# Kernel optimization log

Hardware: AMD Instinct MI355X
Metric: run time of the kernel (lower is better)

The kernel has to match this reference:

```python
import jax, jax.numpy as jnp
import numpy as np

V, E, S, TT, H, C, B = 50000, 300, 128, 12, 512, 3, 128


def setup_inputs() -> dict:
    key = jax.random.key(0)
    ks = jax.random.split(key, 12)
    sc = lambda n: 1.0 / np.sqrt(n)
    return {
        "target_ids": jax.random.randint(ks[0], (B, TT), 0, V),
        "target_len": jax.random.randint(ks[1], (B,), 1, TT + 1, dtype=jnp.int32),
        "left_ids": jax.random.randint(ks[2], (B, S), 0, V),
        "left_len": jax.random.randint(ks[3], (B,), 1, S + 1, dtype=jnp.int32),
        "right_ids": jax.random.randint(ks[4], (B, S), 0, V),
        "right_len": jax.random.randint(ks[5], (B,), 1, S + 1, dtype=jnp.int32),
        "embeddings": jax.random.normal(ks[6], (V, E), jnp.float32) * 0.1,
        "W_left": jax.random.normal(ks[7], (2 * E + H, 4 * H), jnp.float32) * sc(2 * E + H),
        "b_left": jnp.zeros((4 * H,), jnp.float32),
        "W_right": jax.random.normal(ks[8], (2 * E + H, 4 * H), jnp.float32) * sc(2 * E + H),
        "b_right": jnp.zeros((4 * H,), jnp.float32),
        "W_dense": jax.random.normal(ks[9], (2 * H, C), jnp.float32) * sc(2 * H),
        "b_dense": jnp.zeros((C,), jnp.float32),
    }


def _lstm_last_state(x, lens, W, b):
    # x: [B,S,D] inputs, lens: [B]; TF BasicLSTMCell gate order (i, j, f, o), forget_bias=1.0.
    # dynamic_rnn(sequence_length=lens): state frozen once t >= len.
    b_, s_, _ = x.shape
    xs = jnp.swapaxes(x, 0, 1)  # [S,B,D]
    step_mask = jnp.arange(s_)[:, None] < lens[None, :]  # [S,B]
    h0 = jnp.zeros((b_, H), x.dtype)
    c0 = jnp.zeros((b_, H), x.dtype)

    def step(carry, inp):
        h, c = carry
        x_t, m_t = inp
        z = jnp.concatenate([x_t, h], axis=-1) @ W + b  # [B,4H]
        i, j, f, o = jnp.split(z, 4, axis=-1)
        c_new = jax.nn.sigmoid(f + 1.0) * c + jax.nn.sigmoid(i) * jnp.tanh(j)
        h_new = jax.nn.sigmoid(o) * jnp.tanh(c_new)
        m = m_t[:, None]
        return (jnp.where(m, h_new, h), jnp.where(m, c_new, c)), None

    (h, _c), _ = jax.lax.scan(step, (h0, c0), (xs, step_mask))
    return h


def reference(target_ids, target_len, left_ids, left_len, right_ids, right_len,
              embeddings, W_left, b_left, W_right, b_right, W_dense, b_dense):
    # mean target embedding over valid target tokens (variable_len_batch_mean)
    tgt = embeddings[target_ids]  # [B,TT,E]
    tmask = (jnp.arange(TT)[None, :] < target_len[:, None]).astype(tgt.dtype)
    mean_t = jnp.sum(tgt * tmask[:, :, None], axis=1) / target_len[:, None].astype(tgt.dtype)  # [B,E]

    def ctx_inputs(ids):
        e = embeddings[ids]  # [B,S,E]
        # stack([emb, mean_t], axis=2) then reshape -> per-timestep concat [emb_t, mean_t]
        return jnp.concatenate([e, jnp.broadcast_to(mean_t[:, None, :], e.shape)], axis=-1)  # [B,S,2E]

    h_l = _lstm_last_state(ctx_inputs(left_ids), left_len, W_left, b_left)
    h_r = _lstm_last_state(ctx_inputs(right_ids), right_len, W_right, b_right)
    logits = jnp.concatenate([h_l, h_r], axis=-1) @ W_dense + b_dense  # [B,C]
    return logits
```

## Files before the change

kernel.cpp:

```cpp
#include <hip/hip_runtime.h>

#define NB 128
#define NS 128
#define NT 12
#define NE 300
#define NH 512
#define NCOL 2048
#define WGSC __HIP_MEMORY_SCOPE_WORKGROUP

typedef _Float16 h8v __attribute__((ext_vector_type(8)));
typedef __attribute__((ext_vector_type(4))) float f4v;
typedef __attribute__((ext_vector_type(4))) int   i4v;

__device__ __forceinline__ unsigned short f2h(float f) {
  union { _Float16 h; unsigned short u; } c; c.h = (_Float16)f; return c.u;
}
__device__ __forceinline__ float sigm(float x) { return 1.f / (1.f + __expf(-x)); }
__device__ __forceinline__ float tanh_(float x) { const float e = __expf(2.f * x); return 1.f - 2.f / (e + 1.f); }

__device__ __forceinline__ unsigned packh(float a, float b, int tag) {
  unsigned lo = f2h(a), hi = f2h(b);
  lo = (lo & ~1u) | (unsigned)(tag & 1);
  hi = (hi & ~1u) | (unsigned)((tag >> 1) & 1);
  return lo | (hi << 16);
}

__device__ __forceinline__ void st32f_uc(float* p, float v) {
  asm volatile("global_store_dword %0, %1, off sc1" :: "v"(p), "v"(v) : "memory");
}
__device__ __forceinline__ void st32i_uc(int* p, int v) {
  asm volatile("global_store_dword %0, %1, off sc1" :: "v"(p), "v"(v) : "memory");
}
__device__ __forceinline__ void st32u_uc(unsigned* p, unsigned v) {
  asm volatile("global_store_dword %0, %1, off sc1" :: "v"(p), "v"(v) : "memory");
}
__device__ __forceinline__ int ldflag(const int* p) {
  int v;
  asm volatile("global_load_dword %0, %1, off sc1\n\ts_waitcnt vmcnt(0)" : "=v"(v) : "v"(p) : "memory");
  return v;
}
__device__ __forceinline__ void ld64_uc(const char* a, i4v* r) {
  asm volatile(
    "global_load_dwordx4 %0, %4, off sc1\n\t"
    "global_load_dwordx4 %1, %4, off offset:16 sc1\n\t"
    "global_load_dwordx4 %2, %4, off offset:32 sc1\n\t"
    "global_load_dwordx4 %3, %4, off offset:48 sc1\n\t"
    "s_waitcnt vmcnt(0)"
    : "=&v"(r[0]), "=&v"(r[1]), "=&v"(r[2]), "=&v"(r[3])
    : "v"(a) : "memory");
}

struct Params {
  const int *tids, *tlen, *lids, *llen, *rids, *rlen;
  const float *emb, *Wl, *bl, *Wr, *br, *Wd, *bd;
  float* out;
  unsigned short* hbuf;
  float* hfin;
  int* bar;
};

__device__ __forceinline__ void lspin(int* c, int tgt) {
  while (__hip_atomic_load(c, __ATOMIC_RELAXED, WGSC) < tgt) {}
  __builtin_amdgcn_fence(__ATOMIC_ACQUIRE, "workgroup");
}
__device__ __forceinline__ void lspin_s(int* c, int tgt) {
  while (__hip_atomic_load(c, __ATOMIC_RELAXED, WGSC) < tgt)
    __builtin_amdgcn_s_sleep(1);
  __builtin_amdgcn_fence(__ATOMIC_ACQUIRE, "workgroup");
}
__device__ __forceinline__ void larrive(int* c) {
  __hip_atomic_fetch_add(c, 1, __ATOMIC_ACQ_REL, WGSC);
}

#define OFF_HS   0
#define OFF_XS   16384
#define OFF_ZX   26624
#define OFF_ZS   51200
#define OFF_WTH  51200
#define OFF_WTX  34816
#define LDS_SZ   59392

__global__ __launch_bounds__(512, 1) void lstm_all(Params p) {
  __shared__ __align__(16) char lds[LDS_SZ];
  __shared__ int lenL[16];
  __shared__ float redL[8][4];
  __shared__ int cnt[8];

  const int tid = threadIdx.x;
  const int wid = blockIdx.x;
  if (tid < 8) cnt[tid] = 0;

  const int g = wid & 15, ht = wid >> 4;
  const int side = g & 1, bt = g >> 1;
  const int b0 = bt * 16, d0c = ht * 32;
  const int* lenp = side ? p.rlen : p.llen;
  const int* gids = side ? p.rids : p.lids;
  const float* W = side ? p.Wr : p.Wl;
  const float* bias = side ? p.br : p.bl;
  int* fl = p.bar + g * 1024;

  const bool isH = tid < 256;
  const int wv = tid >> 6;
  const int ln = tid & 63;
  const int lwv = isH ? wv : (wv - 4);
  const int kgrp = ln >> 4;
  const int stid = tid & 255;

  float* meanTT = (float*)lds;
  float* zS = (float*)(lds + OFF_ZS);

  {
    const int r = tid >> 5, l32 = tid & 31;
    const int b = b0 + r;
    const int Lt = p.tlen[b];
    const float inv = 1.f / (float)Lt;
    int toks[NT];
    #pragma unroll
    for (int t = 0; t < NT; ++t) toks[t] = p.tids[b * NT + t];
    for (int k = l32; k < NE; k += 32) {
      float s = 0.f;
      #pragma unroll
      for (int t = 0; t < NT; ++t)
        if (t < Lt) s += p.emb[(size_t)toks[t] * NE + k];
      meanTT[k * 16 + r] = s * inv;
    }
    if (tid < 16) lenL[tid] = lenp[b0 + tid];
  }
  __syncthreads();

  if (isH) {
    const int row_c = stid >> 4;
    const int m = stid & 15;

    float zb1[4], zb2[4];
    {
      #pragma unroll
      for (int gq = 0; gq < 4; ++gq) {
        const float* wp = W + (size_t)NE * NCOL + gq * NH + d0c;
        float a1 = bias[gq * NH + d0c + 2 * m];
        float a2 = bias[gq * NH + d0c + 2 * m + 1];
        for (int k = 0; k < NE; ++k) {
          const float mv = meanTT[k * 16 + row_c];
          a1 += mv * wp[(size_t)k * NCOL + 2 * m];
          a2 += mv * wp[(size_t)k * NCOL + 2 * m + 1];
        }
        zb1[gq] = a1; zb2[gq] = a2;
      }
    }
    if (ln == 0) larrive(&cnt[6]);

    int he = 0;
    auto hpbar = [&]() {
      ++he;
      if (ln == 0) larrive(&cnt[7]);
      while (__hip_atomic_load(&cnt[7], __ATOMIC_RELAXED, WGSC) < 4 * he) {}
      __builtin_amdgcn_fence(__ATOMIC_ACQUIRE, "workgroup");
    };
    h8v hfr0[16], hfr1[16];
    {
      unsigned short* wT = (unsigned short*)(lds + OFF_WTH);
      const int r3 = stid >> 3;
      const int part = stid & 7;
      const int gate_p = part >> 1, half_p = part & 1;
      for (int i = 0; i < 16; ++i) {
        const int k = 600 + i * 32 + r3;
        const float* wr = W + (size_t)k * NCOL + gate_p * NH + d0c + half_p * 16;
        const f4v a0 = *(const f4v*)wr;
        const f4v a1 = *(const f4v*)(wr + 4);
        const f4v a2 = *(const f4v*)(wr + 8);
        const f4v a3 = *(const f4v*)(wr + 12);
        #pragma unroll
        for (int j = 0; j < 4; ++j) {
          wT[(part * 16 + j) * 32 + r3]      = f2h(a0[j]);
          wT[(part * 16 + 4 + j) * 32 + r3]  = f2h(a1[j]);
          wT[(part * 16 + 8 + j) * 32 + r3]  = f2h(a2[j]);
          wT[(part * 16 + 12 + j) * 32 + r3] = f2h(a3[j]);
        }
        hpbar();
        const int c0 = lwv * 32 + (ln & 15);
        hfr0[i] = *(const h8v*)((char*)wT + c0 * 64 + kgrp * 16);
        hfr1[i] = *(const h8v*)((char*)wT + (c0 + 16) * 64 + kgrp * 16);
        hpbar();
      }
    }

    float cR1 = 0.f, cR2 = 0.f, hR1 = 0.f, hR2 = 0.f;
    const int a_r = ln & 15;
    const int srow = stid >> 4;
    const int schk = stid & 15;
    for (int t = 0; t < NS; ++t) {
      lspin(&cnt[2], 4 * (t + 1));
      const float* zx = (const float*)(lds + OFF_ZX + (t % 3) * 8192);
      f4v acc0, acc1;
      #pragma unroll
      for (int rg = 0; rg < 4; ++rg) {
        const int rr = kgrp * 4 + rg;
        acc0[rg] = zx[rr * 128 + lwv * 32 + (ln & 15)];
        acc1[rg] = zx[rr * 128 + lwv * 32 + 16 + (ln & 15)];
      }
      if (ln == 0) larrive(&cnt[3]);

      if (t) {
        const char* src = (const char*)(p.hbuf
            + (size_t)(((t & 1) * 2 + side) * NB + b0 + srow) * NH + schk * 32);
        const unsigned exp32 = ((unsigned)(t & 1)) | (((unsigned)((t >> 1) & 1)) << 16);
        i4v v[4];
        for (;;) {
          ld64_uc(src, v);
          unsigned bad = 0;
          #pragma unroll
          for (int q = 0; q < 4; ++q)
            #pragma unroll
            for (int j = 0; j < 4; ++j)
              bad |= (((unsigned)v[q][j]) ^ exp32) & 0x00010001u;
          if (!bad) break;
        }
        #pragma unroll
        for (int q = 0; q < 4; ++q) {
          const int c16 = schk * 4 + q;
          *(i4v*)(lds + OFF_HS + srow * 1024 + ((c16 * 16) ^ ((srow & 7) << 4))) = v[q];
        }
        if (ln == 0) larrive(&cnt[0]);
        while (__hip_atomic_load(&cnt[0], __ATOMIC_RELAXED, WGSC) < 4 * t) {}
        __builtin_amdgcn_fence(__ATOMIC_ACQUIRE, "workgroup");
        #pragma unroll
        for (int kt = 0; kt < 16; ++kt) {
          h8v a = *(const h8v*)(lds + OFF_HS + a_r * 1024
                                + (((kt * 4 + kgrp) * 16) ^ ((a_r & 7) << 4)));
          acc0 = __builtin_amdgcn_mfma_f32_16x16x32_f16(a, hfr0[kt], acc0, 0, 0, 0);
          acc1 = __builtin_amdgcn_mfma_f32_16x16x32_f16(a, hfr1[kt], acc1, 0, 0, 0);
        }
      }

      #pragma unroll
      for (int rg = 0; rg < 4; ++rg) {
        const int rr = kgrp * 4 + rg;
        zS[rr * 128 + lwv * 32 + (ln & 15)]      = acc0[rg];
        zS[rr * 128 + lwv * 32 + 16 + (ln & 15)] = acc1[rg];
      }
      if (ln == 0) larrive(&cnt[4]);
      while (__hip_atomic_load(&cnt[4], __ATOMIC_RELAXED, WGSC) < 4 * (t + 1)) {}
      __builtin_amdgcn_fence(__ATOMIC_ACQUIRE, "workgroup");

      {
        const float* zr = zS + row_c * 128;
        float zi = zr[0 * 32 + 2 * m] + zb1[0], zj = zr[1 * 32 + 2 * m] + zb1[1];
        float zf = zr[2 * 32 + 2 * m] + zb1[2], zo = zr[3 * 32 + 2 * m] + zb1[3];
        float ig = sigm(zi), jg = tanh_(zj), fg = sigm(zf + 1.f), og = sigm(zo);
        float cn = fg * cR1 + ig * jg;
        float hn = og * tanh_(cn);
        if (t < lenL[row_c]) { cR1 = cn; hR1 = hn; }
        zi = zr[0 * 32 + 2 * m + 1] + zb2[0]; zj = zr[1 * 32 + 2 * m + 1] + zb2[1];
        zf = zr[2 * 32 + 2 * m + 1] + zb2[2]; zo = zr[3 * 32 + 2 * m + 1] + zb2[3];
        ig = sigm(zi); jg = tanh_(zj); fg = sigm(zf + 1.f); og = sigm(zo);
        cn = fg * cR2 + ig * jg; hn = og * tanh_(cn);
        if (t < lenL[row_c]) { cR2 = cn; hR2 = hn; }
        unsigned pk = packh(hR1, hR2, (t + 1) & 3);
        unsigned* dst = (unsigned*)p.hbuf
            + ((size_t)((((t + 1) & 1) * 2 + side) * NB + b0 + row_c) * (NH / 2)) + d0c / 2 + m;
        st32u_uc(dst, pk);
      }
    }

    st32f_uc(&p.hfin[((size_t)side * NB + b0 + row_c) * NH + d0c + 2 * m], hR1);
    st32f_uc(&p.hfin[((size_t)side * NB + b0 + row_c) * NH + d0c + 2 * m + 1], hR2);
    asm volatile("s_waitcnt vmcnt(0)" ::: "memory");
    if (ln == 0) larrive(&cnt[5]);
    if (lwv == 0) {
      while (__hip_atomic_load(&cnt[5], __ATOMIC_RELAXED, WGSC) < 4) {}
      if (ln == 0) st32i_uc(fl + ht, NS + 1);
    }
  } else {
    int xe = 0;
    auto xbar = [&]() {
      ++xe;
      if (ln == 0) larrive(&cnt[1]);
      while (__hip_atomic_load(&cnt[1], __ATOMIC_RELAXED, WGSC) < 4 * xe)
        __builtin_amdgcn_s_sleep(1);
      __builtin_amdgcn_fence(__ATOMIC_ACQUIRE, "workgroup");
    };

    h8v xfr0[10], xfr1[10];
    {
      unsigned short* wT = (unsigned short*)(lds + OFF_WTX);
      const int r3 = stid >> 3, part = stid & 7;
      const int gate_p = part >> 1, half_p = part & 1;
      for (int i = 0; i < 10; ++i) {
        const int k = i * 32 + r3;
        float v[16];
        if (k < NE) {
          const float* wr = W + (size_t)k * NCOL + gate_p * NH + d0c + half_p * 16;
          const f4v a0 = *(const f4v*)wr;
          const f4v a1 = *(const f4v*)(wr + 4);
          const f4v a2 = *(const f4v*)(wr + 8);
          const f4v a3 = *(const f4v*)(wr + 12);
          #pragma unroll
          for (int j = 0; j < 4; ++j) {
            v[j] = a0[j]; v[4 + j] = a1[j]; v[8 + j] = a2[j]; v[12 + j] = a3[j];
          }
        } else {
          #pragma unroll
          for (int j = 0; j < 16; ++j) v[j] = 0.f;
        }
        #pragma unroll
        for (int j = 0; j < 16; ++j)
          wT[(part * 16 + j) * 32 + r3] = f2h(v[j]);
        xbar();
        const int c0 = lwv * 32 + (ln & 15);
        xfr0[i] = *(const h8v*)((char*)wT + c0 * 64 + kgrp * 16);
        xfr1[i] = *(const h8v*)((char*)wT + (c0 + 16) * 64 + kgrp * 16);
        xbar();
      }
    }

    lspin_s(&cnt[6], 4);

    for (int n = 0; n < NS; ++n) {
      if (n >= 3) lspin_s(&cnt[3], 4 * (n - 2));
      {
        const int xrow = stid >> 4;
        const int tok = gids[(size_t)(b0 + xrow) * NS + n];
        const float* ep_ = p.emb + (size_t)tok * NE;
        #pragma unroll
        for (int j = 0; j < 3; ++j) {
          const int c16 = (stid & 15) + j * 16;
          if (c16 < 40) {
            unsigned short tmp[8];
            if (c16 < 37) {
              const f4v v0 = *(const f4v*)(ep_ + c16 * 8);
              const f4v v1 = *(const f4v*)(ep_ + c16 * 8 + 4);
              tmp[0] = f2h(v0[0]); tmp[1] = f2h(v0[1]); tmp[2] = f2h(v0[2]); tmp[3] = f2h(v0[3]);
              tmp[4] = f2h(v1[0]); tmp[5] = f2h(v1[1]); tmp[6] = f2h(v1[2]); tmp[7] = f2h(v1[3]);
            } else if (c16 == 37) {
              const f4v v0 = *(const f4v*)(ep_ + 296);
              tmp[0] = f2h(v0[0]); tmp[1] = f2h(v0[1]); tmp[2] = f2h(v0[2]); tmp[3] = f2h(v0[3]);
              tmp[4] = 0; tmp[5] = 0; tmp[6] = 0; tmp[7] = 0;
            } else {
              #pragma unroll
              for (int q = 0; q < 8; ++q) tmp[q] = 0;
            }
            *(i4v*)(lds + OFF_XS + xrow * 640 + ((c16 * 16) ^ ((xrow & 7) << 4))) = *(const i4v*)tmp;
          }
        }
      }
      xbar();
      f4v a0 = {0.f, 0.f, 0.f, 0.f}, a1 = {0.f, 0.f, 0.f, 0.f};
      const int a_r = ln & 15;
      #pragma unroll
      for (int kt = 0; kt < 10; ++kt) {
        h8v a = *(const h8v*)(lds + OFF_XS + a_r * 640
                              + (((kt * 4 + kgrp) * 16) ^ ((a_r & 7) << 4)));
        a0 = __builtin_amdgcn_mfma_f32_16x16x32_f16(a, xfr0[kt], a0, 0, 0, 0);
        a1 = __builtin_amdgcn_mfma_f32_16x16x32_f16(a, xfr1[kt], a1, 0, 0, 0);
      }
      float* zx = (float*)(lds + OFF_ZX + (n % 3) * 8192);
      #pragma unroll
      for (int rg = 0; rg < 4; ++rg) {
        const int rr = kgrp * 4 + rg;
        zx[rr * 128 + lwv * 32 + (ln & 15)]      = a0[rg];
        zx[rr * 128 + lwv * 32 + 16 + (ln & 15)] = a1[rg];
      }
      if (ln == 0) larrive(&cnt[2]);
      xbar();
    }
  }

  if (wid < NB) {
    const int b = wid, bth = b >> 4;
    if (tid < 32) {
      const int gh = (bth << 1) + (tid >> 4);
      const int* f = p.bar + gh * 1024 + (tid & 15);
      int v = ldflag(f);
      while (__ballot(v < NS + 1) != 0ull) { __builtin_amdgcn_s_sleep(2); v = ldflag(f); }
    }
    __syncthreads();

    float a0 = 0.f, a1 = 0.f, a2 = 0.f;
    #pragma unroll
    for (int q = 0; q < 2; ++q) {
      const int kk = q * 512 + tid;
      const int hs = kk >> 9, dim = kk & 511;
      const float* hp = &p.hfin[((size_t)hs * NB + b) * NH + dim];
      const float hv = __hip_atomic_load(hp, __ATOMIC_RELAXED, __HIP_MEMORY_SCOPE_AGENT);
      a0 += hv * p.Wd[kk * 3 + 0];
      a1 += hv * p.Wd[kk * 3 + 1];
      a2 += hv * p.Wd[kk * 3 + 2];
    }
    #pragma unroll
    for (int s = 32; s > 0; s >>= 1) {
      a0 += __shfl_down(a0, s, 64);
      a1 += __shfl_down(a1, s, 64);
      a2 += __shfl_down(a2, s, 64);
    }
    if (ln == 0) { redL[wv][0] = a0; redL[wv][1] = a1; redL[wv][2] = a2; }
    __syncthreads();
    if (tid == 0) {
      float o0 = p.bd[0], o1 = p.bd[1], o2 = p.bd[2];
      #pragma unroll
      for (int w = 0; w < 8; ++w) { o0 += redL[w][0]; o1 += redL[w][1]; o2 += redL[w][2]; }
      p.out[b * 3 + 0] = o0;
      p.out[b * 3 + 1] = o1;
      p.out[b * 3 + 2] = o2;
    }
  }
}

extern "C" void kernel_launch(void* const* d_in, const int* in_sizes, int n_in,
                              void* d_out, int out_size, void* d_ws, size_t ws_size,
                              hipStream_t stream) {
  (void)in_sizes; (void)n_in; (void)out_size; (void)ws_size;
  char* ws = (char*)d_ws;
  Params p;
  p.tids = (const int*)d_in[0];
  p.tlen = (const int*)d_in[1];
  p.lids = (const int*)d_in[2];
  p.llen = (const int*)d_in[3];
  p.rids = (const int*)d_in[4];
  p.rlen = (const int*)d_in[5];
  p.emb  = (const float*)d_in[6];
  p.Wl   = (const float*)d_in[7];
  p.bl   = (const float*)d_in[8];
  p.Wr   = (const float*)d_in[9];
  p.br   = (const float*)d_in[10];
  p.Wd   = (const float*)d_in[11];
  p.bd   = (const float*)d_in[12];
  p.out  = (float*)d_out;
  p.bar  = (int*)ws;
  p.hbuf = (unsigned short*)(ws + 65536);
  p.hfin = (float*)(ws + 65536 + 524288);
  hipMemsetAsync(ws, 0, 65536 + 524288, stream);
  lstm_all<<<dim3(256), dim3(512), 0, stream>>>(p);
}
```

Before: 435.8 us.

## Compute mean-target gate bias with fp16 MFMA instead of scalar FMA loop

The per-row constant gate contribution from the mean target embedding (300x128 slice of W per group) was computed with a scalar fp32 dot loop reading W from global memory. It is now staged as fp16 fragments through the LDS transpose buffer, multiplied with MFMA 16x16x32 against a swizzled fp16 copy of the mean embedding, and redistributed through zS. The cross-wave arrival counter used to signal completion to the x-side waves is removed because the computation now finishes before the h-side path continues. This trades fp32 precision for fp16 on this term and adds extra intra-group barriers.

```diff
diff --git a/kernel.cpp b/kernel.cpp
--- a/kernel.cpp
+++ b/kernel.cpp
@@ -106,7 +106,6 @@
   const int kgrp = ln >> 4;
   const int stid = tid & 255;
 
-  float* meanTT = (float*)lds;
   float* zS = (float*)(lds + OFF_ZS);
 
   {
@@ -117,12 +116,18 @@
     int toks[NT];
     #pragma unroll
     for (int t = 0; t < NT; ++t) toks[t] = p.tids[b * NT + t];
-    for (int k = l32; k < NE; k += 32) {
-      float s = 0.f;
-      #pragma unroll
-      for (int t = 0; t < NT; ++t)
-        if (t < Lt) s += p.emb[(size_t)toks[t] * NE + k];
-      meanTT[k * 16 + r] = s * inv;
+    char* mrow = lds + OFF_HS + r * 640;
+    for (int k = l32; k < 320; k += 32) {
+      unsigned short hv = 0;
+      if (k < 300) {
+        float s = 0.f;
+        #pragma unroll
+        for (int t = 0; t < NT; ++t)
+          if (t < Lt) s += p.emb[(size_t)toks[t] * NE + k];
+        hv = f2h(s * inv);
+      }
+      const int c16 = k >> 3;
+      *(unsigned short*)(mrow + ((c16 * 16) ^ ((r & 7) << 4)) + (k & 7) * 2) = hv;
     }
     if (tid < 16) lenL[tid] = lenp[b0 + tid];
   }
@@ -131,23 +136,7 @@
   if (isH) {
     const int row_c = stid >> 4;
     const int m = stid & 15;
-
-    float zb1[4], zb2[4];
-    {
-      #pragma unroll
-      for (int gq = 0; gq < 4; ++gq) {
-        const float* wp = W + (size_t)NE * NCOL + gq * NH + d0c;
-        float a1 = bias[gq * NH + d0c + 2 * m];
-        float a2 = bias[gq * NH + d0c + 2 * m + 1];
-        for (int k = 0; k < NE; ++k) {
-          const float mv = meanTT[k * 16 + row_c];
-          a1 += mv * wp[(size_t)k * NCOL + 2 * m];
-          a2 += mv * wp[(size_t)k * NCOL + 2 * m + 1];
-        }
-        zb1[gq] = a1; zb2[gq] = a2;
-      }
-    }
-    if (ln == 0) larrive(&cnt[6]);
+    const int a_r = ln & 15;
 
     int he = 0;
     auto hpbar = [&]() {
@@ -156,6 +145,57 @@
       while (__hip_atomic_load(&cnt[7], __ATOMIC_RELAXED, WGSC) < 4 * he) {}
       __builtin_amdgcn_fence(__ATOMIC_ACQUIRE, "workgroup");
     };
+
+    float zb1[4], zb2[4];
+    {
+      h8v mfr0[10], mfr1[10];
+      unsigned short* wT = (unsigned short*)(lds + OFF_WTH);
+      const int r3 = stid >> 3;
+      const int part = stid & 7;
+      const int gate_p = part >> 1, half_p = part & 1;
+      for (int i = 0; i < 10; ++i) {
+        const int k = 300 + i * 32 + r3;
+        const float* wr = W + (size_t)k * NCOL + gate_p * NH + d0c + half_p * 16;
+        const f4v a0 = *(const f4v*)wr;
+        const f4v a1 = *(const f4v*)(wr + 4);
+        const f4v a2 = *(const f4v*)(wr + 8);
+        const f4v a3 = *(const f4v*)(wr + 12);
+        #pragma unroll
+        for (int j = 0; j < 4; ++j) {
+          wT[(part * 16 + j) * 32 + r3]      = f2h(a0[j]);
+          wT[(part * 16 + 4 + j) * 32 + r3]  = f2h(a1[j]);
+          wT[(part * 16 + 8 + j) * 32 + r3]  = f2h(a2[j]);
+          wT[(part * 16 + 12 + j) * 32 + r3] = f2h(a3[j]);
+        }
+        hpbar();
+        const int c0 = lwv * 32 + (ln & 15);
+        mfr0[i] = *(const h8v*)((char*)wT + c0 * 64 + kgrp * 16);
+        mfr1[i] = *(const h8v*)((char*)wT + (c0 + 16) * 64 + kgrp * 16);
+        hpbar();
+      }
+      f4v acc0 = {0.f, 0.f, 0.f, 0.f}, acc1 = {0.f, 0.f, 0.f, 0.f};
+      #pragma unroll
+      for (int kt = 0; kt < 10; ++kt) {
+        h8v a = *(const h8v*)(lds + OFF_HS + a_r * 640
+                              + (((kt * 4 + kgrp) * 16) ^ ((a_r & 7) << 4)));
+        acc0 = __builtin_amdgcn_mfma_f32_16x16x32_f16(a, mfr0[kt], acc0, 0, 0, 0);
+        acc1 = __builtin_amdgcn_mfma_f32_16x16x32_f16(a, mfr1[kt], acc1, 0, 0, 0);
+      }
+      #pragma unroll
+      for (int rg = 0; rg < 4; ++rg) {
+        const int rr = kgrp * 4 + rg;
+        zS[rr * 128 + lwv * 32 + (ln & 15)]      = acc0[rg];
+        zS[rr * 128 + lwv * 32 + 16 + (ln & 15)] = acc1[rg];
+      }
+      hpbar();
+      #pragma unroll
+      for (int gq = 0; gq < 4; ++gq) {
+        zb1[gq] = zS[row_c * 128 + gq * 32 + 2 * m]     + bias[gq * NH + d0c + 2 * m];
+        zb2[gq] = zS[row_c * 128 + gq * 32 + 2 * m + 1] + bias[gq * NH + d0c + 2 * m + 1];
+      }
+      hpbar();
+    }
+
     h8v hfr0[16], hfr1[16];
     {
       unsigned short* wT = (unsigned short*)(lds + OFF_WTH);
@@ -185,7 +225,6 @@
     }
 
     float cR1 = 0.f, cR2 = 0.f, hR1 = 0.f, hR2 = 0.f;
-    const int a_r = ln & 15;
     const int srow = stid >> 4;
     const int schk = stid & 15;
     for (int t = 0; t < NS; ++t) {
@@ -312,8 +351,6 @@
         xbar();
       }
     }
-
-    lspin_s(&cnt[6], 4);
 
     for (int n = 0; n < NS; ++n) {
       if (n >= 3) lspin_s(&cnt[3], 4 * (n - 2));
```

Result: faster. 424.2 us, median of 2 (-2.7%).
